# Optimization experiments

Hardware: AMD Instinct MI355X
Metric: run time of the kernel (lower is better)

Reference implementation:

```python
import jax, jax.numpy as jnp
import numpy as np
import math

C_S = 256
NUM_HEADS = 8
HEAD_DIM = 32
TOTAL = NUM_HEADS * HEAD_DIM
B, S, I = 1, 256, 256  # batch, msa sequences (column attn axis), residues
LN_EPS = 1e-5


def setup_inputs() -> dict:
    key = jax.random.key(0)
    ks = jax.random.split(key, 10)
    sc = 1.0 / math.sqrt(C_S)
    return {
        "msa": jax.random.normal(ks[0], (B, S, I, C_S), dtype=jnp.float32),
        "ln_gamma": jnp.ones((C_S,), dtype=jnp.float32),
        "ln_beta": jnp.zeros((C_S,), dtype=jnp.float32),
        "Wq": jax.random.normal(ks[1], (C_S, TOTAL), dtype=jnp.float32) * sc,
        "Wk": jax.random.normal(ks[2], (C_S, TOTAL), dtype=jnp.float32) * sc,
        "Wv": jax.random.normal(ks[3], (C_S, TOTAL), dtype=jnp.float32) * sc,
        "Wg": jax.random.normal(ks[4], (C_S, TOTAL), dtype=jnp.float32) * sc,
        "bg": jnp.zeros((TOTAL,), dtype=jnp.float32),
        "Wo": jax.random.normal(ks[5], (TOTAL, C_S), dtype=jnp.float32) * (1.0 / math.sqrt(TOTAL)),
        "bo": jnp.zeros((C_S,), dtype=jnp.float32),
    }


def reference(msa, ln_gamma, ln_beta, Wq, Wk, Wv, Wg, bg, Wo, bo):
    # LayerNorm over channel dim
    mu = jnp.mean(msa, axis=-1, keepdims=True)
    var = jnp.mean(jnp.square(msa - mu), axis=-1, keepdims=True)
    x = (msa - mu) * jax.lax.rsqrt(var + LN_EPS) * ln_gamma + ln_beta

    b, s, i, _ = x.shape
    hd = (NUM_HEADS, HEAD_DIM)
    Q = (x @ Wq).reshape(b, s, i, *hd)
    K = (x @ Wk).reshape(b, s, i, *hd)
    V = (x @ Wv).reshape(b, s, i, *hd)
    G = jax.nn.sigmoid((x @ Wg + bg).reshape(b, s, i, *hd))

    # column attention: contract over head_dim, attend over sequence axis s/t
    scores = jnp.einsum('bsihd,btihd->bihst', Q, K) / math.sqrt(HEAD_DIM)
    attn = jax.nn.softmax(scores, axis=-1)
    vals = jnp.einsum('bihst,btihd->bsihd', attn, V)

    vals = (G * vals).reshape(b, s, i, TOTAL)
    return vals @ Wo + bo
```

## Files before the change

kernel.cpp:

```cpp
#include <hip/hip_runtime.h>
#include <hip/hip_fp16.h>
#include <math.h>

#define C_S 256
#define NUM_HEADS 8
#define HEAD_DIM 32
#define TOTAL 256
#define S_DIM 256
#define I_DIM 256
#define NROWS (S_DIM * I_DIM)
#define LN_EPS 1e-5f
#define QSCALE 0.25503534f

typedef _Float16 f16x8 __attribute__((ext_vector_type(8)));
typedef __attribute__((ext_vector_type(4))) float f32x4;

__device__ __forceinline__ ushort f2h(float x) {
  return __half_as_ushort(__float2half(x));
}
__device__ __forceinline__ float h2f(ushort u) {
  return __half2float(__ushort_as_half(u));
}
__device__ __forceinline__ void gl16(const void* g, void* l) {
  __builtin_amdgcn_global_load_lds(
      (const __attribute__((address_space(1))) unsigned*)g,
      (__attribute__((address_space(3))) unsigned*)l, 16, 0, 0);
}

__global__ __launch_bounds__(256) void prep_w_kernel(
    const float* __restrict__ Wq, const float* __restrict__ Wk,
    const float* __restrict__ Wv, const float* __restrict__ Wg,
    const float* __restrict__ Wo,
    ushort* __restrict__ Wch, ushort* __restrict__ Woh) {
  const int b = blockIdx.x;
  const int mat = b >> 8, n = b & 255;
  const int k = threadIdx.x;
  const float* W = (mat == 0) ? Wq : (mat == 1) ? Wk
                  : (mat == 2) ? Wv : (mat == 3) ? Wg : Wo;
  ushort h = f2h(W[(size_t)k * 256 + n]);
  if (mat < 4) Wch[((size_t)(mat * 256 + n)) * 256 + k] = h;
  else         Woh[(size_t)n * 256 + k] = h;
}

__global__ __launch_bounds__(256) void prep_x_kernel(
    const float* __restrict__ msa, const float* __restrict__ gamma,
    const float* __restrict__ beta, ushort* __restrict__ Xh) {
  const int row  = blockIdx.x * 4 + (threadIdx.x >> 6);
  const int lane = threadIdx.x & 63;
  float4 v = ((const float4*)(msa + (size_t)row * C_S))[lane];
  float sum = v.x + v.y + v.z + v.w;
  float sq  = v.x*v.x + v.y*v.y + v.z*v.z + v.w*v.w;
  #pragma unroll
  for (int off = 1; off < 64; off <<= 1) {
    sum += __shfl_xor(sum, off);
    sq  += __shfl_xor(sq, off);
  }
  float mu = sum * (1.0f / 256.0f);
  float rs = rsqrtf(sq * (1.0f / 256.0f) - mu * mu + LN_EPS);
  float4 gv = ((const float4*)gamma)[lane];
  float4 bv = ((const float4*)beta)[lane];
  ushort4 hh;
  hh.x = f2h((v.x - mu) * rs * gv.x + bv.x);
  hh.y = f2h((v.y - mu) * rs * gv.y + bv.y);
  hh.z = f2h((v.z - mu) * rs * gv.z + bv.z);
  hh.w = f2h((v.w - mu) * rs * gv.w + bv.w);
  *(ushort4*)(Xh + (size_t)row * 256 + lane * 4) = hh;
}

__global__ __launch_bounds__(256, 2) void fused_attn_kernel(
    const ushort* __restrict__ Xh,
    const ushort* __restrict__ Wch,
    const float* __restrict__ bg,
    ushort* __restrict__ Oh) {
  __shared__ __align__(16) ushort Kls[256][40];
  __shared__ __align__(16) ushort Vth[32][264];
  __shared__ __align__(16) ushort PQ[256][72];

  const int bid = blockIdx.x;
  const int xcd = bid & 7, j = bid >> 3;
  const int h = j & 7;
  const int i = (xcd << 5) + (j >> 3);
  const int ih = i * NUM_HEADS + h;
  const int tid = threadIdx.x;
  const int wave = tid >> 6, lane = tid & 63;
  const int lr = lane & 15, quad = lane >> 4;
  const int s_base = wave * 64;
  const size_t hbase = (size_t)ih * (S_DIM * HEAD_DIM);

  const ushort* xr0 = Xh + ((size_t)(s_base + lr) * 256 + i) * 256 + quad * 8;
  const ushort* wr0 = Wch + ((size_t)(h * 32 + lr)) * 256 + quad * 8;

  f32x4 kacc[2][4] = {}, vacc[2][4] = {};
  #pragma unroll
  for (int kb = 0; kb < 8; ++kb) {
    f16x8 xb[4];
    #pragma unroll
    for (int nt = 0; nt < 4; ++nt)
      xb[nt] = *(const f16x8*)(xr0 + (size_t)nt * 16 * 65536 + kb * 32);
    f16x8 wk[2], wv[2];
    #pragma unroll
    for (int mt = 0; mt < 2; ++mt) {
      wk[mt] = *(const f16x8*)(wr0 + (size_t)1 * 65536 + mt * 4096 + kb * 32);
      wv[mt] = *(const f16x8*)(wr0 + (size_t)2 * 65536 + mt * 4096 + kb * 32);
    }
    #pragma unroll
    for (int mt = 0; mt < 2; ++mt)
      #pragma unroll
      for (int nt = 0; nt < 4; ++nt) {
        kacc[mt][nt] = __builtin_amdgcn_mfma_f32_16x16x32_f16(wk[mt], xb[nt], kacc[mt][nt], 0, 0, 0);
        vacc[mt][nt] = __builtin_amdgcn_mfma_f32_16x16x32_f16(wv[mt], xb[nt], vacc[mt][nt], 0, 0, 0);
      }
  }
  #pragma unroll
  for (int mt = 0; mt < 2; ++mt)
    #pragma unroll
    for (int nt = 0; nt < 4; ++nt) {
      const int t = s_base + nt * 16 + lr;
      ushort4 kp;
      kp.x = f2h(kacc[mt][nt][0]); kp.y = f2h(kacc[mt][nt][1]);
      kp.z = f2h(kacc[mt][nt][2]); kp.w = f2h(kacc[mt][nt][3]);
      *(ushort4*)&Kls[t][mt * 16 + quad * 4] = kp;
      #pragma unroll
      for (int reg = 0; reg < 4; ++reg)
        Vth[mt * 16 + quad * 4 + reg][t] = f2h(vacc[mt][nt][reg]);
    }

  f32x4 qacc[2][4] = {}, gacc[2][4] = {};
  #pragma unroll
  for (int kb = 0; kb < 8; ++kb) {
    f16x8 xb[4];
    #pragma unroll
    for (int nt = 0; nt < 4; ++nt)
      xb[nt] = *(const f16x8*)(xr0 + (size_t)nt * 16 * 65536 + kb * 32);
    f16x8 wq[2], wg[2];
    #pragma unroll
    for (int mt = 0; mt < 2; ++mt) {
      wq[mt] = *(const f16x8*)(wr0 + (size_t)0 * 65536 + mt * 4096 + kb * 32);
      wg[mt] = *(const f16x8*)(wr0 + (size_t)3 * 65536 + mt * 4096 + kb * 32);
    }
    #pragma unroll
    for (int mt = 0; mt < 2; ++mt)
      #pragma unroll
      for (int nt = 0; nt < 4; ++nt) {
        qacc[mt][nt] = __builtin_amdgcn_mfma_f32_16x16x32_f16(wq[mt], xb[nt], qacc[mt][nt], 0, 0, 0);
        gacc[mt][nt] = __builtin_amdgcn_mfma_f32_16x16x32_f16(wg[mt], xb[nt], gacc[mt][nt], 0, 0, 0);
      }
  }
  #pragma unroll
  for (int mt = 0; mt < 2; ++mt)
    #pragma unroll
    for (int nt = 0; nt < 4; ++nt) {
      const int s = s_base + nt * 16 + lr;
      ushort4 qp;
      qp.x = f2h(qacc[mt][nt][0] * QSCALE); qp.y = f2h(qacc[mt][nt][1] * QSCALE);
      qp.z = f2h(qacc[mt][nt][2] * QSCALE); qp.w = f2h(qacc[mt][nt][3] * QSCALE);
      *(ushort4*)&PQ[s][mt * 16 + quad * 4] = qp;
    }
  f16x8 qf[4];
  #pragma unroll
  for (int ns = 0; ns < 4; ++ns)
    qf[ns] = *(const f16x8*)&PQ[s_base + ns * 16 + lr][quad * 8];
  f32x4 gv[2][4];
  #pragma unroll
  for (int mt = 0; mt < 2; ++mt) {
    float4 bgv = *(const float4*)(bg + h * 32 + mt * 16 + quad * 4);
    float bga[4] = {bgv.x, bgv.y, bgv.z, bgv.w};
    #pragma unroll
    for (int nt = 0; nt < 4; ++nt)
      #pragma unroll
      for (int reg = 0; reg < 4; ++reg)
        gv[mt][nt][reg] = 1.0f / (1.0f + __expf(-(gacc[mt][nt][reg] + bga[reg])));
  }

  __syncthreads();

  f32x4 oacc[2][4] = {};
  float lpart[4] = {};
  #pragma unroll 1
  for (int c = 0; c < 4; ++c) {
    const int t0 = c * 64;
    f16x8 kf[4];
    #pragma unroll
    for (int mt = 0; mt < 4; ++mt)
      kf[mt] = *(const f16x8*)&Kls[t0 + mt * 16 + lr][quad * 8];
    #pragma unroll
    for (int mt = 0; mt < 4; ++mt) {
      #pragma unroll
      for (int ns = 0; ns < 4; ++ns) {
        f32x4 sc = {};
        sc = __builtin_amdgcn_mfma_f32_16x16x32_f16(kf[mt], qf[ns], sc, 0, 0, 0);
        ushort u0 = f2h(exp2f(sc[0])), u1 = f2h(exp2f(sc[1]));
        ushort u2 = f2h(exp2f(sc[2])), u3 = f2h(exp2f(sc[3]));
        lpart[ns] += (h2f(u0) + h2f(u1)) + (h2f(u2) + h2f(u3));
        ushort4 pk = make_ushort4(u0, u1, u2, u3);
        *(ushort4*)&PQ[s_base + ns * 16 + lr][mt * 16 + quad * 4] = pk;
      }
    }
    #pragma unroll
    for (int ks = 0; ks < 2; ++ks) {
      const int tq = t0 + ks * 32 + quad * 8;
      f16x8 v0 = *(const f16x8*)&Vth[lr][tq];
      f16x8 v1 = *(const f16x8*)&Vth[16 + lr][tq];
      #pragma unroll
      for (int ns = 0; ns < 4; ++ns) {
        f16x8 pf = *(const f16x8*)&PQ[s_base + ns * 16 + lr][ks * 32 + quad * 8];
        oacc[0][ns] = __builtin_amdgcn_mfma_f32_16x16x32_f16(v0, pf, oacc[0][ns], 0, 0, 0);
        oacc[1][ns] = __builtin_amdgcn_mfma_f32_16x16x32_f16(v1, pf, oacc[1][ns], 0, 0, 0);
      }
    }
  }

  float invl[4];
  #pragma unroll
  for (int ns = 0; ns < 4; ++ns) {
    float v = lpart[ns];
    v += __shfl_xor(v, 16);
    v += __shfl_xor(v, 32);
    invl[ns] = 1.0f / v;
  }

  #pragma unroll
  for (int ns = 0; ns < 4; ++ns) {
    const int s = s_base + ns * 16 + lr;
    #pragma unroll
    for (int md = 0; md < 2; ++md) {
      const int d0 = md * 16 + quad * 4;
      ushort4 ov;
      ov.x = f2h(gv[md][ns][0] * oacc[md][ns][0] * invl[ns]);
      ov.y = f2h(gv[md][ns][1] * oacc[md][ns][1] * invl[ns]);
      ov.z = f2h(gv[md][ns][2] * oacc[md][ns][2] * invl[ns]);
      ov.w = f2h(gv[md][ns][3] * oacc[md][ns][3] * invl[ns]);
      *(ushort4*)(Oh + hbase + (size_t)s * HEAD_DIM + d0) = ov;
    }
  }
}

__global__ __launch_bounds__(256) void out_kernel(
    const ushort* __restrict__ Oh, const ushort* __restrict__ Woh,
    const float* __restrict__ bo, float* __restrict__ out) {
  __shared__ __align__(16) ushort At0[128 * 32];
  __shared__ __align__(16) ushort At1[128 * 32];
  __shared__ __align__(16) ushort Bt0[128 * 32];
  __shared__ __align__(16) ushort Bt1[128 * 32];

  const int bid = blockIdx.x;
  const int xcd = bid & 7;
  const int j   = bid >> 3;
  const int ntile = j & 1;
  const int rg    = (xcd << 6) + (j >> 1);
  const int n0 = ntile * 128;
  const int s  = rg >> 1;
  const int i0 = (rg & 1) * 128;
  const int tid = threadIdx.x;
  const int wave = tid >> 6, lane = tid & 63;
  const int wm = wave >> 1, wn = wave & 1;
  const int lr = lane & 15, quad = lane >> 4;
  const int fsw = (quad ^ ((lr >> 1) & 3)) * 8;

  const int slot = wave * 64 + lane;
  const int row0 = slot >> 2;
  const int kc   = ((slot & 3) ^ ((row0 >> 1) & 3)) * 8;

  const ushort* pA = Oh + (size_t)(i0 + row0) * 65536 + (size_t)s * 32 + kc;
  const ushort* pB = Woh + (size_t)(n0 + row0) * 256 + kc;
  const int ld0 = wave * 512;
  const int ld1 = 2048 + wave * 512;

  f32x4 acc[4][4] = {};

  for (int kk = 0; kk < 4; ++kk) {
    __syncthreads();
    gl16(pA,               At0 + ld0); gl16(pA + (size_t)64 * 65536,        At0 + ld1);
    gl16(pA + 8192,        At1 + ld0); gl16(pA + (size_t)64 * 65536 + 8192, At1 + ld1);
    gl16(pB,               Bt0 + ld0); gl16(pB + 64 * 256,                  Bt0 + ld1);
    gl16(pB + 32,          Bt1 + ld0); gl16(pB + 64 * 256 + 32,             Bt1 + ld1);
    pA += 16384;
    pB += 64;
    __syncthreads();

    f16x8 a0[4], a1[4], b0[4], b1[4];
    #pragma unroll
    for (int mt = 0; mt < 4; ++mt) {
      const int off = (wm * 64 + mt * 16 + lr) * 32 + fsw;
      a0[mt] = *(const f16x8*)&At0[off];
      a1[mt] = *(const f16x8*)&At1[off];
    }
    #pragma unroll
    for (int nt = 0; nt < 4; ++nt) {
      const int off = (wn * 64 + nt * 16 + lr) * 32 + fsw;
      b0[nt] = *(const f16x8*)&Bt0[off];
      b1[nt] = *(const f16x8*)&Bt1[off];
    }
    #pragma unroll
    for (int mt = 0; mt < 4; ++mt)
      #pragma unroll
      for (int nt = 0; nt < 4; ++nt) {
        acc[mt][nt] = __builtin_amdgcn_mfma_f32_16x16x32_f16(a0[mt], b0[nt], acc[mt][nt], 0, 0, 0);
        acc[mt][nt] = __builtin_amdgcn_mfma_f32_16x16x32_f16(a1[mt], b1[nt], acc[mt][nt], 0, 0, 0);
      }
  }

  #pragma unroll
  for (int nt = 0; nt < 4; ++nt) {
    const int col = n0 + wn * 64 + nt * 16 + lr;
    const float b = bo[col];
    #pragma unroll
    for (int mt = 0; mt < 4; ++mt)
      #pragma unroll
      for (int reg = 0; reg < 4; ++reg) {
        const int mloc = wm * 64 + mt * 16 + quad * 4 + reg;
        out[((size_t)s * 256 + i0 + mloc) * C_S + col] = acc[mt][nt][reg] + b;
      }
  }
}

extern "C" void kernel_launch(void* const* d_in, const int* in_sizes, int n_in,
                              void* d_out, int out_size, void* d_ws, size_t ws_size,
                              hipStream_t stream) {
  const float* msa   = (const float*)d_in[0];
  const float* gamma = (const float*)d_in[1];
  const float* beta  = (const float*)d_in[2];
  const float* Wq    = (const float*)d_in[3];
  const float* Wk    = (const float*)d_in[4];
  const float* Wv    = (const float*)d_in[5];
  const float* Wg    = (const float*)d_in[6];
  const float* bg    = (const float*)d_in[7];
  const float* Wo    = (const float*)d_in[8];
  const float* bo    = (const float*)d_in[9];
  float* out = (float*)d_out;

  const size_t PLANE = (size_t)NROWS * TOTAL;
  ushort* Oh  = (ushort*)d_ws;
  ushort* Wch = Oh + PLANE;
  ushort* Woh = Wch + 1024 * 256;
  ushort* Xh = (ushort*)d_out;

  prep_w_kernel<<<1280, 256, 0, stream>>>(Wq, Wk, Wv, Wg, Wo, Wch, Woh);
  prep_x_kernel<<<NROWS / 4, 256, 0, stream>>>(msa, gamma, beta, Xh);
  fused_attn_kernel<<<I_DIM * NUM_HEADS, 256, 0, stream>>>(Xh, Wch, bg, Oh);
  out_kernel<<<1024, 256, 0, stream>>>(Oh, Woh, bo, out);
}
```

Measured before the change: 286.1 us.

## Shrink P/Q LDS buffer with swizzle, vectorize V transpose store, raise occupancy

Swaps the MFMA operands for V so V^T can be written to LDS as packed ushort4 stores instead of scalar transposed stores. Replaces the 256x72 PQ buffer with a 256x32 buffer using an XOR swizzle, processing P in 32-column halves interleaved with the PV MFMAs. The smaller LDS footprint allows launch bounds to request three blocks per CU. The row sum now accumulates fp32 exps instead of rounded fp16 values, and the higher occupancy target may force register spills.

```diff
diff --git a/kernel.cpp b/kernel.cpp
--- a/kernel.cpp
+++ b/kernel.cpp
@@ -67,14 +67,14 @@
   *(ushort4*)(Xh + (size_t)row * 256 + lane * 4) = hh;
 }
 
-__global__ __launch_bounds__(256, 2) void fused_attn_kernel(
+__global__ __launch_bounds__(256, 3) void fused_attn_kernel(
     const ushort* __restrict__ Xh,
     const ushort* __restrict__ Wch,
     const float* __restrict__ bg,
     ushort* __restrict__ Oh) {
   __shared__ __align__(16) ushort Kls[256][40];
   __shared__ __align__(16) ushort Vth[32][264];
-  __shared__ __align__(16) ushort PQ[256][72];
+  __shared__ __align__(16) ushort Pls[256][32];
 
   const int bid = blockIdx.x;
   const int xcd = bid & 7, j = bid >> 3;
@@ -87,6 +87,10 @@
   const int s_base = wave * 64;
   const size_t hbase = (size_t)ih * (S_DIM * HEAD_DIM);
 
+  const int lrb0 = lr & 1, lrb1 = (lr >> 1) & 1;
+  const int qw  = quad ^ (lrb0 << 1);
+  const int prd = (quad ^ (lr & 3)) << 3;
+
   const ushort* xr0 = Xh + ((size_t)(s_base + lr) * 256 + i) * 256 + quad * 8;
   const ushort* wr0 = Wch + ((size_t)(h * 32 + lr)) * 256 + quad * 8;
 
@@ -108,7 +112,7 @@
       #pragma unroll
       for (int nt = 0; nt < 4; ++nt) {
         kacc[mt][nt] = __builtin_amdgcn_mfma_f32_16x16x32_f16(wk[mt], xb[nt], kacc[mt][nt], 0, 0, 0);
-        vacc[mt][nt] = __builtin_amdgcn_mfma_f32_16x16x32_f16(wv[mt], xb[nt], vacc[mt][nt], 0, 0, 0);
+        vacc[mt][nt] = __builtin_amdgcn_mfma_f32_16x16x32_f16(xb[nt], wv[mt], vacc[mt][nt], 0, 0, 0);
       }
   }
   #pragma unroll
@@ -120,9 +124,10 @@
       kp.x = f2h(kacc[mt][nt][0]); kp.y = f2h(kacc[mt][nt][1]);
       kp.z = f2h(kacc[mt][nt][2]); kp.w = f2h(kacc[mt][nt][3]);
       *(ushort4*)&Kls[t][mt * 16 + quad * 4] = kp;
-      #pragma unroll
-      for (int reg = 0; reg < 4; ++reg)
-        Vth[mt * 16 + quad * 4 + reg][t] = f2h(vacc[mt][nt][reg]);
+      ushort4 vp;
+      vp.x = f2h(vacc[mt][nt][0]); vp.y = f2h(vacc[mt][nt][1]);
+      vp.z = f2h(vacc[mt][nt][2]); vp.w = f2h(vacc[mt][nt][3]);
+      *(ushort4*)&Vth[mt * 16 + lr][s_base + nt * 16 + quad * 4] = vp;
     }
 
   f32x4 qacc[2][4] = {}, gacc[2][4] = {};
@@ -147,19 +152,21 @@
       }
   }
   #pragma unroll
-  for (int mt = 0; mt < 2; ++mt)
+  for (int mt = 0; mt < 2; ++mt) {
+    const int cw = ((mt ^ lrb1) << 4) + (qw << 2);
     #pragma unroll
     for (int nt = 0; nt < 4; ++nt) {
       const int s = s_base + nt * 16 + lr;
       ushort4 qp;
       qp.x = f2h(qacc[mt][nt][0] * QSCALE); qp.y = f2h(qacc[mt][nt][1] * QSCALE);
       qp.z = f2h(qacc[mt][nt][2] * QSCALE); qp.w = f2h(qacc[mt][nt][3] * QSCALE);
-      *(ushort4*)&PQ[s][mt * 16 + quad * 4] = qp;
-    }
+      *(ushort4*)&Pls[s][cw] = qp;
+    }
+  }
   f16x8 qf[4];
   #pragma unroll
   for (int ns = 0; ns < 4; ++ns)
-    qf[ns] = *(const f16x8*)&PQ[s_base + ns * 16 + lr][quad * 8];
+    qf[ns] = *(const f16x8*)&Pls[s_base + ns * 16 + lr][prd];
   f32x4 gv[2][4];
   #pragma unroll
   for (int mt = 0; mt < 2; ++mt) {
@@ -184,26 +191,29 @@
     for (int mt = 0; mt < 4; ++mt)
       kf[mt] = *(const f16x8*)&Kls[t0 + mt * 16 + lr][quad * 8];
     #pragma unroll
-    for (int mt = 0; mt < 4; ++mt) {
-      #pragma unroll
-      for (int ns = 0; ns < 4; ++ns) {
-        f32x4 sc = {};
-        sc = __builtin_amdgcn_mfma_f32_16x16x32_f16(kf[mt], qf[ns], sc, 0, 0, 0);
-        ushort u0 = f2h(exp2f(sc[0])), u1 = f2h(exp2f(sc[1]));
-        ushort u2 = f2h(exp2f(sc[2])), u3 = f2h(exp2f(sc[3]));
-        lpart[ns] += (h2f(u0) + h2f(u1)) + (h2f(u2) + h2f(u3));
-        ushort4 pk = make_ushort4(u0, u1, u2, u3);
-        *(ushort4*)&PQ[s_base + ns * 16 + lr][mt * 16 + quad * 4] = pk;
-      }
-    }
-    #pragma unroll
-    for (int ks = 0; ks < 2; ++ks) {
-      const int tq = t0 + ks * 32 + quad * 8;
+    for (int half = 0; half < 2; ++half) {
+      #pragma unroll
+      for (int m2 = 0; m2 < 2; ++m2) {
+        const int mt = half * 2 + m2;
+        const int cw = ((m2 ^ lrb1) << 4) + (qw << 2);
+        #pragma unroll
+        for (int ns = 0; ns < 4; ++ns) {
+          f32x4 sc = {};
+          sc = __builtin_amdgcn_mfma_f32_16x16x32_f16(kf[mt], qf[ns], sc, 0, 0, 0);
+          float e0 = exp2f(sc[0]), e1 = exp2f(sc[1]);
+          float e2 = exp2f(sc[2]), e3 = exp2f(sc[3]);
+          lpart[ns] += (e0 + e1) + (e2 + e3);
+          ushort4 pk;
+          pk.x = f2h(e0); pk.y = f2h(e1); pk.z = f2h(e2); pk.w = f2h(e3);
+          *(ushort4*)&Pls[s_base + ns * 16 + lr][cw] = pk;
+        }
+      }
+      const int tq = t0 + half * 32 + quad * 8;
       f16x8 v0 = *(const f16x8*)&Vth[lr][tq];
       f16x8 v1 = *(const f16x8*)&Vth[16 + lr][tq];
       #pragma unroll
       for (int ns = 0; ns < 4; ++ns) {
-        f16x8 pf = *(const f16x8*)&PQ[s_base + ns * 16 + lr][ks * 32 + quad * 8];
+        f16x8 pf = *(const f16x8*)&Pls[s_base + ns * 16 + lr][prd];
         oacc[0][ns] = __builtin_amdgcn_mfma_f32_16x16x32_f16(v0, pf, oacc[0][ns], 0, 0, 0);
         oacc[1][ns] = __builtin_amdgcn_mfma_f32_16x16x32_f16(v1, pf, oacc[1][ns], 0, 0, 0);
       }
```

Result: no change. 282.3 us (-1.3%).
